# Kernel tuning notes

Hardware: AMD Instinct MI355X
Metric: run time of the kernel (lower is better)

## Reference

```python
import jax, jax.numpy as jnp
import numpy as np

EPS = 1e-7  # keras K.epsilon()


def setup_inputs() -> dict:
    key = jax.random.key(0)
    k1, k2, k3, k4 = jax.random.split(key, 4)
    B, Lc, La, Dc, Da = 64, 512, 64, 1024, 1024
    return {
        "context": jax.random.normal(k1, (B, Lc, Dc), dtype=jnp.float32),
        "asp_text": jax.random.normal(k2, (B, La, Da), dtype=jnp.float32),
        "context_w": jax.random.normal(k3, (Dc, Da), dtype=jnp.float32) / np.sqrt(Dc),
        "context_b": jnp.zeros((Lc,), dtype=jnp.float32),
        "aspect_w": jax.random.normal(k4, (Da, Dc), dtype=jnp.float32) / np.sqrt(Da),
        "aspect_b": jnp.zeros((La,), dtype=jnp.float32),
    }


def reference(context, asp_text, context_w, context_b, aspect_w, aspect_b):
    # context: [B, Lc, Dc], asp_text: [B, La, Da]
    context_avg = jnp.mean(context, axis=1)   # [B, Dc]
    asp_avg = jnp.mean(asp_text, axis=1)      # [B, Da]

    # context attention scored against mean-pooled aspect
    s_c = jnp.einsum('bld,de,be->bl', context, context_w, asp_avg)  # [B, Lc]
    a_c = jnp.exp(jnp.tanh(s_c + context_b))
    a_c = a_c / (jnp.sum(a_c, axis=1, keepdims=True) + EPS)
    attend_context = jnp.einsum('bld,bl->bd', context, a_c)         # [B, Dc]

    # aspect attention scored against mean-pooled context
    s_t = jnp.einsum('bld,de,be->bl', asp_text, aspect_w, context_avg)  # [B, La]
    a_t = jnp.exp(jnp.tanh(s_t + aspect_b))
    # NOTE: faithful to original code's bug -- a_t is REPLACED by its sum
    # (not normalized), so the aspect branch scales sum(asp_text) by a scalar.
    a_t_sum = jnp.sum(a_t, axis=1, keepdims=True) + EPS              # [B, 1]
    attend_asp = jnp.sum(asp_text * a_t_sum[..., None], axis=1)      # [B, Da]

    return jnp.concatenate([attend_context, attend_asp], axis=-1)    # [B, Dc+Da]
```

## Files before the change

### kernel.cpp

```cpp
#include <hip/hip_runtime.h>
#include <hip/hip_bf16.h>

#define EPS 1e-7f

#define B   64
#define LC  512
#define LA  64
#define D   1024
#define D4  256
#define CHUNKS 32
#define ROWS_PER_CHUNK (LC / CHUNKS)

__global__ void k_asp_mean(const float* __restrict__ A, float* __restrict__ avg) {
    int b  = blockIdx.y;
    int f4 = blockIdx.x * 64 + threadIdx.x;
    const float4* base = reinterpret_cast<const float4*>(A + (size_t)b * LA * D);
    float sx = 0.f, sy = 0.f, sz = 0.f, sw = 0.f;
    #pragma unroll 8
    for (int l = 0; l < LA; ++l) {
        float4 v = base[l * D4 + f4];
        sx += v.x; sy += v.y; sz += v.z; sw += v.w;
    }
    const float inv = 1.0f / (float)LA;
    float4 o; o.x = sx * inv; o.y = sy * inv; o.z = sz * inv; o.w = sw * inv;
    reinterpret_cast<float4*>(avg)[b * D4 + f4] = o;
}

__global__ void k_matvec_rows(const float* __restrict__ W, const float* __restrict__ X,
                              float* __restrict__ V) {
    __shared__ float xrow[D];
    int w    = threadIdx.x >> 6;
    int lane = threadIdx.x & 63;
    int d    = blockIdx.x * 4 + w;

    float4 wr[4];
    const float4* Wrow = reinterpret_cast<const float4*>(W + (size_t)d * D);
    #pragma unroll
    for (int k = 0; k < 4; ++k) wr[k] = Wrow[lane + 64 * k];

    for (int b = 0; b < B; ++b) {
        __syncthreads();
        reinterpret_cast<float4*>(xrow)[threadIdx.x] =
            reinterpret_cast<const float4*>(X + (size_t)b * D)[threadIdx.x];
        __syncthreads();
        float p = 0.f;
        #pragma unroll
        for (int k = 0; k < 4; ++k) {
            float4 x = reinterpret_cast<const float4*>(xrow)[lane + 64 * k];
            p += wr[k].x * x.x + wr[k].y * x.y + wr[k].z * x.z + wr[k].w * x.w;
        }
        #pragma unroll
        for (int m = 1; m < 64; m <<= 1) p += __shfl_xor(p, m, 64);
        if (lane == 0) V[b * D + d] = p;
    }
}

__global__ void k_ctx_pass(const float* __restrict__ C, const float* __restrict__ vc,
                           const float* __restrict__ cb,
                           float* __restrict__ pacc, float* __restrict__ psum,
                           float* __restrict__ pesum) {
    int b    = blockIdx.y;
    int c    = blockIdx.x;
    int lane = threadIdx.x;

    float4 vr[4];
    const float4* vcr = reinterpret_cast<const float4*>(vc + (size_t)b * D);
    #pragma unroll
    for (int k = 0; k < 4; ++k) vr[k] = vcr[lane + 64 * k];

    float4 acc[4], sct[4];
    #pragma unroll
    for (int k = 0; k < 4; ++k) {
        acc[k].x = acc[k].y = acc[k].z = acc[k].w = 0.f;
        sct[k].x = sct[k].y = sct[k].z = sct[k].w = 0.f;
    }
    float esum = 0.f;

    const float4* Cb = reinterpret_cast<const float4*>(C + (size_t)b * LC * D);
    for (int r = 0; r < ROWS_PER_CHUNK; ++r) {
        int l = c * ROWS_PER_CHUNK + r;
        const float4* row = Cb + (size_t)l * D4;
        float4 x[4];
        #pragma unroll
        for (int k = 0; k < 4; ++k) x[k] = row[lane + 64 * k];
        float p = 0.f;
        #pragma unroll
        for (int k = 0; k < 4; ++k)
            p += x[k].x * vr[k].x + x[k].y * vr[k].y + x[k].z * vr[k].z + x[k].w * vr[k].w;
        #pragma unroll
        for (int m = 1; m < 64; m <<= 1) p += __shfl_xor(p, m, 64);
        float e = expf(tanhf(p + cb[l]));
        esum += e;
        #pragma unroll
        for (int k = 0; k < 4; ++k) {
            acc[k].x += e * x[k].x; acc[k].y += e * x[k].y;
            acc[k].z += e * x[k].z; acc[k].w += e * x[k].w;
            sct[k].x += x[k].x; sct[k].y += x[k].y;
            sct[k].z += x[k].z; sct[k].w += x[k].w;
        }
    }

    int pidx = b * CHUNKS + c;
    float4* pa = reinterpret_cast<float4*>(pacc + (size_t)pidx * D);
    float4* ps = reinterpret_cast<float4*>(psum + (size_t)pidx * D);
    #pragma unroll
    for (int k = 0; k < 4; ++k) { pa[lane + 64 * k] = acc[k]; ps[lane + 64 * k] = sct[k]; }
    if (lane == 0) pesum[pidx] = esum;
}

__global__ void k_ctx_reduce(const float* __restrict__ pacc, const float* __restrict__ psum,
                             const float* __restrict__ pesum,
                             float* __restrict__ out, float* __restrict__ ctx_avg) {
    int b = blockIdx.x;
    int t = threadIdx.x;
    float ax = 0.f, ay = 0.f, az = 0.f, aw = 0.f;
    float sx = 0.f, sy = 0.f, sz = 0.f, sw = 0.f;
    for (int c = 0; c < CHUNKS; ++c) {
        const float4* pa = reinterpret_cast<const float4*>(pacc + (size_t)(b * CHUNKS + c) * D);
        const float4* ps = reinterpret_cast<const float4*>(psum + (size_t)(b * CHUNKS + c) * D);
        float4 va = pa[t], vs = ps[t];
        ax += va.x; ay += va.y; az += va.z; aw += va.w;
        sx += vs.x; sy += vs.y; sz += vs.z; sw += vs.w;
    }
    float es = 0.f;
    for (int c = 0; c < CHUNKS; ++c) es += pesum[b * CHUNKS + c];
    float inv = 1.0f / (es + EPS);
    float4 o; o.x = ax * inv; o.y = ay * inv; o.z = az * inv; o.w = aw * inv;
    reinterpret_cast<float4*>(out)[b * (2 * D4) + t] = o;
    const float invL = 1.0f / (float)LC;
    float4 m; m.x = sx * invL; m.y = sy * invL; m.z = sz * invL; m.w = sw * invL;
    reinterpret_cast<float4*>(ctx_avg)[b * D4 + t] = m;
}

__global__ void k_asp_pass(const float* __restrict__ A, const float* __restrict__ vt,
                           const float* __restrict__ ab, const float* __restrict__ asp_avg,
                           float* __restrict__ out) {
    __shared__ float wsum[4];
    int b    = blockIdx.x;
    int w    = threadIdx.x >> 6;
    int lane = threadIdx.x & 63;

    float4 vr[4];
    const float4* vtr = reinterpret_cast<const float4*>(vt + (size_t)b * D);
    #pragma unroll
    for (int k = 0; k < 4; ++k) vr[k] = vtr[lane + 64 * k];

    float esum = 0.f;
    const float4* Ab = reinterpret_cast<const float4*>(A + (size_t)b * LA * D);
    for (int r = 0; r < 16; ++r) {
        int l = w * 16 + r;
        const float4* row = Ab + (size_t)l * D4;
        float p = 0.f;
        #pragma unroll
        for (int k = 0; k < 4; ++k) {
            float4 x = row[lane + 64 * k];
            p += x.x * vr[k].x + x.y * vr[k].y + x.z * vr[k].z + x.w * vr[k].w;
        }
        #pragma unroll
        for (int m = 1; m < 64; m <<= 1) p += __shfl_xor(p, m, 64);
        esum += expf(tanhf(p + ab[l]));
    }
    if (lane == 0) wsum[w] = esum;
    __syncthreads();
    float scale = (wsum[0] + wsum[1] + wsum[2] + wsum[3] + EPS) * (float)LA;
    float4 av = reinterpret_cast<const float4*>(asp_avg)[b * D4 + threadIdx.x];
    float4 o; o.x = av.x * scale; o.y = av.y * scale; o.z = av.z * scale; o.w = av.w * scale;
    reinterpret_cast<float4*>(out)[b * (2 * D4) + D4 + threadIdx.x] = o;
}

extern "C" void kernel_launch(void* const* d_in, const int* in_sizes, int n_in,
                              void* d_out, int out_size, void* d_ws, size_t ws_size,
                              hipStream_t stream) {
    const float* context   = (const float*)d_in[0];
    const float* asp_text  = (const float*)d_in[1];
    const float* context_w = (const float*)d_in[2];
    const float* context_b = (const float*)d_in[3];
    const float* aspect_w  = (const float*)d_in[4];
    const float* aspect_b  = (const float*)d_in[5];
    float* out = (float*)d_out;
    float* ws  = (float*)d_ws;

    float* asp_avg = ws;
    float* v_c     = asp_avg + B * D;
    float* ctx_avg = v_c + B * D;
    float* v_t     = ctx_avg + B * D;
    float* pacc    = v_t + B * D;
    float* psum    = pacc + B * CHUNKS * D;
    float* pesum   = psum + B * CHUNKS * D;

    k_asp_mean<<<dim3(4, B), 64, 0, stream>>>(asp_text, asp_avg);
    k_matvec_rows<<<D / 4, 256, 0, stream>>>(context_w, asp_avg, v_c);
    k_ctx_pass<<<dim3(CHUNKS, B), 64, 0, stream>>>(context, v_c, context_b,
                                                   pacc, psum, pesum);
    k_ctx_reduce<<<B, 256, 0, stream>>>(pacc, psum, pesum, out, ctx_avg);
    k_matvec_rows<<<D / 4, 256, 0, stream>>>(aspect_w, ctx_avg, v_t);
    k_asp_pass<<<B, 256, 0, stream>>>(asp_text, v_t, aspect_b, asp_avg, out);
}
```

Baseline: 319.2 us.

## Restructure all kernels for more parallelism and wider blocks across pipeline stages

The context pass now uses 256-thread blocks where each wave handles a quarter of the feature dimension over 16 rows. All 16 rows are loaded up front, and per-row dot products are combined through shared memory. The matvec now computes two weight rows per wave over a 16-batch slice on a 2D grid, with no shared-memory staging or per-batch barriers. The aspect mean and aspect scoring are each split into a partial kernel plus a combine or scale kernel, and the context reduction is split across feature quarters. The aim is to raise occupancy and memory-level parallelism on the bandwidth-bound passes, at the cost of extra launches and larger partial buffers.

```diff
diff --git a/kernel.cpp b/kernel.cpp
--- a/kernel.cpp
+++ b/kernel.cpp
@@ -8,164 +8,190 @@
 #define LA  64
 #define D   1024
 #define D4  256
-#define CHUNKS 32
-#define ROWS_PER_CHUNK (LC / CHUNKS)
-
-__global__ void k_asp_mean(const float* __restrict__ A, float* __restrict__ avg) {
-    int b  = blockIdx.y;
-    int f4 = blockIdx.x * 64 + threadIdx.x;
-    const float4* base = reinterpret_cast<const float4*>(A + (size_t)b * LA * D);
+#define ROWS 16
+#define CCHUNKS (LC / ROWS)
+
+__global__ void k_asp_psum(const float* __restrict__ A, float* __restrict__ P) {
+    int b = blockIdx.y, s = blockIdx.x, t = threadIdx.x;
+    const float4* Ab = reinterpret_cast<const float4*>(A + (size_t)b * LA * D);
     float sx = 0.f, sy = 0.f, sz = 0.f, sw = 0.f;
-    #pragma unroll 8
-    for (int l = 0; l < LA; ++l) {
-        float4 v = base[l * D4 + f4];
+    #pragma unroll
+    for (int r = 0; r < ROWS; ++r) {
+        float4 v = Ab[(s * ROWS + r) * D4 + t];
+        sx += v.x; sy += v.y; sz += v.z; sw += v.w;
+    }
+    float4 o; o.x = sx; o.y = sy; o.z = sz; o.w = sw;
+    reinterpret_cast<float4*>(P)[(b * 4 + s) * D4 + t] = o;
+}
+
+__global__ void k_asp_combine(const float* __restrict__ P, float* __restrict__ avg) {
+    int b = blockIdx.x, t = threadIdx.x;
+    const float4* P4 = reinterpret_cast<const float4*>(P);
+    float sx = 0.f, sy = 0.f, sz = 0.f, sw = 0.f;
+    #pragma unroll
+    for (int s = 0; s < 4; ++s) {
+        float4 v = P4[(b * 4 + s) * D4 + t];
         sx += v.x; sy += v.y; sz += v.z; sw += v.w;
     }
     const float inv = 1.0f / (float)LA;
     float4 o; o.x = sx * inv; o.y = sy * inv; o.z = sz * inv; o.w = sw * inv;
-    reinterpret_cast<float4*>(avg)[b * D4 + f4] = o;
-}
-
-__global__ void k_matvec_rows(const float* __restrict__ W, const float* __restrict__ X,
-                              float* __restrict__ V) {
-    __shared__ float xrow[D];
+    reinterpret_cast<float4*>(avg)[b * D4 + t] = o;
+}
+
+__global__ void k_matvec(const float* __restrict__ W, const float* __restrict__ X,
+                         float* __restrict__ V) {
     int w    = threadIdx.x >> 6;
     int lane = threadIdx.x & 63;
-    int d    = blockIdx.x * 4 + w;
-
-    float4 wr[4];
-    const float4* Wrow = reinterpret_cast<const float4*>(W + (size_t)d * D);
-    #pragma unroll
-    for (int k = 0; k < 4; ++k) wr[k] = Wrow[lane + 64 * k];
-
-    for (int b = 0; b < B; ++b) {
-        __syncthreads();
-        reinterpret_cast<float4*>(xrow)[threadIdx.x] =
-            reinterpret_cast<const float4*>(X + (size_t)b * D)[threadIdx.x];
-        __syncthreads();
-        float p = 0.f;
+    int d0   = (blockIdx.x * 4 + w) * 2;
+    int b0   = blockIdx.y * 16;
+
+    float4 w0[4], w1[4];
+    const float4* Wr0 = reinterpret_cast<const float4*>(W + (size_t)d0 * D);
+    const float4* Wr1 = reinterpret_cast<const float4*>(W + (size_t)(d0 + 1) * D);
+    #pragma unroll
+    for (int k = 0; k < 4; ++k) { w0[k] = Wr0[lane + 64 * k]; w1[k] = Wr1[lane + 64 * k]; }
+
+    #pragma unroll 4
+    for (int bb = 0; bb < 16; ++bb) {
+        int b = b0 + bb;
+        const float4* Xr = reinterpret_cast<const float4*>(X + (size_t)b * D);
+        float p0 = 0.f, p1 = 0.f;
         #pragma unroll
         for (int k = 0; k < 4; ++k) {
-            float4 x = reinterpret_cast<const float4*>(xrow)[lane + 64 * k];
-            p += wr[k].x * x.x + wr[k].y * x.y + wr[k].z * x.z + wr[k].w * x.w;
+            float4 x = Xr[lane + 64 * k];
+            p0 += x.x * w0[k].x + x.y * w0[k].y + x.z * w0[k].z + x.w * w0[k].w;
+            p1 += x.x * w1[k].x + x.y * w1[k].y + x.z * w1[k].z + x.w * w1[k].w;
         }
         #pragma unroll
+        for (int m = 1; m < 64; m <<= 1) {
+            p0 += __shfl_xor(p0, m, 64);
+            p1 += __shfl_xor(p1, m, 64);
+        }
+        if (lane == 0) { V[b * D + d0] = p0; V[b * D + d0 + 1] = p1; }
+    }
+}
+
+__global__ __launch_bounds__(256, 4)
+void k_ctx_pass(const float* __restrict__ C, const float* __restrict__ vc,
+                const float* __restrict__ cb,
+                float* __restrict__ pacc, float* __restrict__ psum,
+                float* __restrict__ pesum) {
+    __shared__ float sdot[ROWS][4];
+    __shared__ float se[ROWS];
+    int b = blockIdx.y, c = blockIdx.x;
+    int w    = threadIdx.x >> 6;
+    int lane = threadIdx.x & 63;
+    int f4   = w * 64 + lane;
+
+    float4 vr = reinterpret_cast<const float4*>(vc + (size_t)b * D)[f4];
+
+    const float4* Cb = reinterpret_cast<const float4*>(C + ((size_t)b * LC + c * ROWS) * D);
+    float4 x[ROWS];
+    #pragma unroll
+    for (int r = 0; r < ROWS; ++r) x[r] = Cb[r * D4 + f4];
+
+    #pragma unroll
+    for (int r = 0; r < ROWS; ++r) {
+        float p = x[r].x * vr.x + x[r].y * vr.y + x[r].z * vr.z + x[r].w * vr.w;
+        #pragma unroll
         for (int m = 1; m < 64; m <<= 1) p += __shfl_xor(p, m, 64);
-        if (lane == 0) V[b * D + d] = p;
-    }
-}
-
-__global__ void k_ctx_pass(const float* __restrict__ C, const float* __restrict__ vc,
-                           const float* __restrict__ cb,
-                           float* __restrict__ pacc, float* __restrict__ psum,
-                           float* __restrict__ pesum) {
-    int b    = blockIdx.y;
-    int c    = blockIdx.x;
-    int lane = threadIdx.x;
-
-    float4 vr[4];
-    const float4* vcr = reinterpret_cast<const float4*>(vc + (size_t)b * D);
-    #pragma unroll
-    for (int k = 0; k < 4; ++k) vr[k] = vcr[lane + 64 * k];
-
-    float4 acc[4], sct[4];
-    #pragma unroll
-    for (int k = 0; k < 4; ++k) {
-        acc[k].x = acc[k].y = acc[k].z = acc[k].w = 0.f;
-        sct[k].x = sct[k].y = sct[k].z = sct[k].w = 0.f;
-    }
-    float esum = 0.f;
-
-    const float4* Cb = reinterpret_cast<const float4*>(C + (size_t)b * LC * D);
-    for (int r = 0; r < ROWS_PER_CHUNK; ++r) {
-        int l = c * ROWS_PER_CHUNK + r;
-        const float4* row = Cb + (size_t)l * D4;
-        float4 x[4];
-        #pragma unroll
-        for (int k = 0; k < 4; ++k) x[k] = row[lane + 64 * k];
-        float p = 0.f;
-        #pragma unroll
-        for (int k = 0; k < 4; ++k)
-            p += x[k].x * vr[k].x + x[k].y * vr[k].y + x[k].z * vr[k].z + x[k].w * vr[k].w;
-        #pragma unroll
-        for (int m = 1; m < 64; m <<= 1) p += __shfl_xor(p, m, 64);
-        float e = expf(tanhf(p + cb[l]));
-        esum += e;
-        #pragma unroll
-        for (int k = 0; k < 4; ++k) {
-            acc[k].x += e * x[k].x; acc[k].y += e * x[k].y;
-            acc[k].z += e * x[k].z; acc[k].w += e * x[k].w;
-            sct[k].x += x[k].x; sct[k].y += x[k].y;
-            sct[k].z += x[k].z; sct[k].w += x[k].w;
-        }
-    }
-
-    int pidx = b * CHUNKS + c;
-    float4* pa = reinterpret_cast<float4*>(pacc + (size_t)pidx * D);
-    float4* ps = reinterpret_cast<float4*>(psum + (size_t)pidx * D);
-    #pragma unroll
-    for (int k = 0; k < 4; ++k) { pa[lane + 64 * k] = acc[k]; ps[lane + 64 * k] = sct[k]; }
-    if (lane == 0) pesum[pidx] = esum;
+        if (lane == 0) sdot[r][w] = p;
+    }
+    __syncthreads();
+    if (threadIdx.x < ROWS) {
+        int r = threadIdx.x;
+        float s = sdot[r][0] + sdot[r][1] + sdot[r][2] + sdot[r][3];
+        se[r] = expf(tanhf(s + cb[c * ROWS + r]));
+    }
+    __syncthreads();
+
+    float4 acc = {0.f, 0.f, 0.f, 0.f}, sct = {0.f, 0.f, 0.f, 0.f};
+    #pragma unroll
+    for (int r = 0; r < ROWS; ++r) {
+        float e = se[r];
+        acc.x += e * x[r].x; acc.y += e * x[r].y; acc.z += e * x[r].z; acc.w += e * x[r].w;
+        sct.x += x[r].x;     sct.y += x[r].y;     sct.z += x[r].z;     sct.w += x[r].w;
+    }
+    int pidx = b * CCHUNKS + c;
+    reinterpret_cast<float4*>(pacc)[pidx * D4 + f4] = acc;
+    reinterpret_cast<float4*>(psum)[pidx * D4 + f4] = sct;
+    if (w == 0) {
+        float e2 = (lane < ROWS) ? se[lane] : 0.f;
+        #pragma unroll
+        for (int m = 1; m < 64; m <<= 1) e2 += __shfl_xor(e2, m, 64);
+        if (lane == 0) pesum[pidx] = e2;
+    }
 }
 
 __global__ void k_ctx_reduce(const float* __restrict__ pacc, const float* __restrict__ psum,
                              const float* __restrict__ pesum,
                              float* __restrict__ out, float* __restrict__ ctx_avg) {
-    int b = blockIdx.x;
-    int t = threadIdx.x;
+    int b = blockIdx.y, q = blockIdx.x;
+    int f4 = q * 64 + threadIdx.x;
     float ax = 0.f, ay = 0.f, az = 0.f, aw = 0.f;
     float sx = 0.f, sy = 0.f, sz = 0.f, sw = 0.f;
-    for (int c = 0; c < CHUNKS; ++c) {
-        const float4* pa = reinterpret_cast<const float4*>(pacc + (size_t)(b * CHUNKS + c) * D);
-        const float4* ps = reinterpret_cast<const float4*>(psum + (size_t)(b * CHUNKS + c) * D);
-        float4 va = pa[t], vs = ps[t];
+    const float4* pa = reinterpret_cast<const float4*>(pacc);
+    const float4* ps = reinterpret_cast<const float4*>(psum);
+    #pragma unroll 8
+    for (int c = 0; c < CCHUNKS; ++c) {
+        float4 va = pa[(b * CCHUNKS + c) * D4 + f4];
+        float4 vs = ps[(b * CCHUNKS + c) * D4 + f4];
         ax += va.x; ay += va.y; az += va.z; aw += va.w;
         sx += vs.x; sy += vs.y; sz += vs.z; sw += vs.w;
     }
     float es = 0.f;
-    for (int c = 0; c < CHUNKS; ++c) es += pesum[b * CHUNKS + c];
+    #pragma unroll 8
+    for (int c = 0; c < CCHUNKS; ++c) es += pesum[b * CCHUNKS + c];
     float inv = 1.0f / (es + EPS);
     float4 o; o.x = ax * inv; o.y = ay * inv; o.z = az * inv; o.w = aw * inv;
-    reinterpret_cast<float4*>(out)[b * (2 * D4) + t] = o;
+    reinterpret_cast<float4*>(out)[b * (2 * D4) + f4] = o;
     const float invL = 1.0f / (float)LC;
     float4 m; m.x = sx * invL; m.y = sy * invL; m.z = sz * invL; m.w = sw * invL;
-    reinterpret_cast<float4*>(ctx_avg)[b * D4 + t] = m;
-}
-
-__global__ void k_asp_pass(const float* __restrict__ A, const float* __restrict__ vt,
-                           const float* __restrict__ ab, const float* __restrict__ asp_avg,
-                           float* __restrict__ out) {
-    __shared__ float wsum[4];
-    int b    = blockIdx.x;
+    reinterpret_cast<float4*>(ctx_avg)[b * D4 + f4] = m;
+}
+
+__global__ void k_asp_score(const float* __restrict__ A, const float* __restrict__ vt,
+                            const float* __restrict__ ab, float* __restrict__ pesumA) {
+    __shared__ float sdot[ROWS][4];
+    __shared__ float se[ROWS];
+    int b = blockIdx.y, q = blockIdx.x;
     int w    = threadIdx.x >> 6;
     int lane = threadIdx.x & 63;
-
-    float4 vr[4];
-    const float4* vtr = reinterpret_cast<const float4*>(vt + (size_t)b * D);
-    #pragma unroll
-    for (int k = 0; k < 4; ++k) vr[k] = vtr[lane + 64 * k];
-
-    float esum = 0.f;
-    const float4* Ab = reinterpret_cast<const float4*>(A + (size_t)b * LA * D);
-    for (int r = 0; r < 16; ++r) {
-        int l = w * 16 + r;
-        const float4* row = Ab + (size_t)l * D4;
-        float p = 0.f;
-        #pragma unroll
-        for (int k = 0; k < 4; ++k) {
-            float4 x = row[lane + 64 * k];
-            p += x.x * vr[k].x + x.y * vr[k].y + x.z * vr[k].z + x.w * vr[k].w;
-        }
+    int f4   = w * 64 + lane;
+
+    float4 vr = reinterpret_cast<const float4*>(vt + (size_t)b * D)[f4];
+    const float4* Ab = reinterpret_cast<const float4*>(A + ((size_t)b * LA + q * ROWS) * D);
+    #pragma unroll
+    for (int r = 0; r < ROWS; ++r) {
+        float4 x = Ab[r * D4 + f4];
+        float p = x.x * vr.x + x.y * vr.y + x.z * vr.z + x.w * vr.w;
         #pragma unroll
         for (int m = 1; m < 64; m <<= 1) p += __shfl_xor(p, m, 64);
-        esum += expf(tanhf(p + ab[l]));
-    }
-    if (lane == 0) wsum[w] = esum;
-    __syncthreads();
-    float scale = (wsum[0] + wsum[1] + wsum[2] + wsum[3] + EPS) * (float)LA;
-    float4 av = reinterpret_cast<const float4*>(asp_avg)[b * D4 + threadIdx.x];
+        if (lane == 0) sdot[r][w] = p;
+    }
+    __syncthreads();
+    if (threadIdx.x < ROWS) {
+        int r = threadIdx.x;
+        float s = sdot[r][0] + sdot[r][1] + sdot[r][2] + sdot[r][3];
+        se[r] = expf(tanhf(s + ab[q * ROWS + r]));
+    }
+    __syncthreads();
+    if (w == 0) {
+        float e2 = (lane < ROWS) ? se[lane] : 0.f;
+        #pragma unroll
+        for (int m = 1; m < 64; m <<= 1) e2 += __shfl_xor(e2, m, 64);
+        if (lane == 0) pesumA[b * 4 + q] = e2;
+    }
+}
+
+__global__ void k_asp_scale(const float* __restrict__ pesumA, const float* __restrict__ asp_avg,
+                            float* __restrict__ out) {
+    int b = blockIdx.x, t = threadIdx.x;
+    float es = pesumA[b * 4 + 0] + pesumA[b * 4 + 1] + pesumA[b * 4 + 2] + pesumA[b * 4 + 3];
+    float scale = (es + EPS) * (float)LA;
+    float4 av = reinterpret_cast<const float4*>(asp_avg)[b * D4 + t];
     float4 o; o.x = av.x * scale; o.y = av.y * scale; o.z = av.z * scale; o.w = av.w * scale;
-    reinterpret_cast<float4*>(out)[b * (2 * D4) + D4 + threadIdx.x] = o;
+    reinterpret_cast<float4*>(out)[b * (2 * D4) + D4 + t] = o;
 }
 
 extern "C" void kernel_launch(void* const* d_in, const int* in_sizes, int n_in,
@@ -185,14 +211,18 @@
     float* ctx_avg = v_c + B * D;
     float* v_t     = ctx_avg + B * D;
     float* pacc    = v_t + B * D;
-    float* psum    = pacc + B * CHUNKS * D;
-    float* pesum   = psum + B * CHUNKS * D;
-
-    k_asp_mean<<<dim3(4, B), 64, 0, stream>>>(asp_text, asp_avg);
-    k_matvec_rows<<<D / 4, 256, 0, stream>>>(context_w, asp_avg, v_c);
-    k_ctx_pass<<<dim3(CHUNKS, B), 64, 0, stream>>>(context, v_c, context_b,
-                                                   pacc, psum, pesum);
-    k_ctx_reduce<<<B, 256, 0, stream>>>(pacc, psum, pesum, out, ctx_avg);
-    k_matvec_rows<<<D / 4, 256, 0, stream>>>(aspect_w, ctx_avg, v_t);
-    k_asp_pass<<<B, 256, 0, stream>>>(asp_text, v_t, aspect_b, asp_avg, out);
-}
+    float* psum    = pacc + (size_t)B * CCHUNKS * D;
+    float* pesum   = psum + (size_t)B * CCHUNKS * D;
+    float* pesumA  = pesum + B * CCHUNKS;
+    float* Ppart   = pesumA + B * 4;
+
+    k_asp_psum   <<<dim3(4, B),  256, 0, stream>>>(asp_text, Ppart);
+    k_asp_combine<<<B,           256, 0, stream>>>(Ppart, asp_avg);
+    k_matvec     <<<dim3(128, 4),256, 0, stream>>>(context_w, asp_avg, v_c);
+    k_ctx_pass   <<<dim3(CCHUNKS, B), 256, 0, stream>>>(context, v_c, context_b,
+                                                        pacc, psum, pesum);
+    k_ctx_reduce <<<dim3(4, B),  64,  0, stream>>>(pacc, psum, pesum, out, ctx_avg);
+    k_matvec     <<<dim3(128, 4),256, 0, stream>>>(aspect_w, ctx_avg, v_t);
+    k_asp_score  <<<dim3(4, B),  256, 0, stream>>>(asp_text, v_t, aspect_b, pesumA);
+    k_asp_scale  <<<B,           256, 0, stream>>>(pesumA, asp_avg, out);
+}
```

Result: faster. 264.6 us (-17.1%).
